# Kernel tuning notes

Hardware: AMD Instinct MI355X
Metric: run time of the kernel (lower is better)

The kernel has to match this reference:

```python
import math
import jax, jax.numpy as jnp
import numpy as np

B, N, F, FE = 16, 24, 128, 128   # crystals, atoms/crystal, atom feat, edge feat
NUM_Z = 100                       # num_atomic_numbers
GAUSS_STOP, BASIS_W = 6.0, 1.0
RADIUS_RATE = 1.0
N_CONV, N_FC, FC_F = 3, 4, 128
REP = 1                           # PBC replication per axis (27 images); exact for our cells
ZDIM = 2 * F + FE


def setup_inputs() -> dict:
    key = jax.random.key(0)
    ks = jax.random.split(key, 12)
    # cubic cells with side length in [8, 10) Angstrom -> rep per axis is exactly 1
    L = 8.0 + 2.0 * jax.random.uniform(ks[0], (B,))
    cell = L[:, None, None] * jnp.eye(3, dtype=jnp.float32)          # [B,3,3]
    frac = jax.random.uniform(ks[1], (B, N, 3))
    pos = jnp.einsum('bnd,bde->bne', frac, cell).reshape(B * N, 3)   # [B*N,3]
    atomic_numbers = jax.random.randint(ks[2], (B * N,), 1, NUM_Z + 1)
    batch = jnp.repeat(jnp.arange(B), N)
    emb = jax.random.normal(ks[3], (NUM_Z, F)) * 0.1                 # embedding table
    s = 1.0 / math.sqrt(ZDIM)
    conv_Wf = jax.random.normal(ks[4], (N_CONV, ZDIM, F)) * s
    conv_bf = jnp.zeros((N_CONV, F))
    conv_Ws = jax.random.normal(ks[5], (N_CONV, ZDIM, F)) * s
    conv_bs = jnp.zeros((N_CONV, F))
    sf = 1.0 / math.sqrt(FC_F)
    fc_W = jax.random.normal(ks[6], (N_FC - 1, FC_F, FC_F)) * sf
    fc_b = jnp.zeros((N_FC - 1, FC_F))
    W_out = jax.random.normal(ks[7], (FC_F, 1)) * sf
    b_out = jnp.zeros((1,))
    return {'pos': pos, 'cell': cell, 'emb': emb,
            'conv_Wf': conv_Wf, 'conv_bf': conv_bf,
            'conv_Ws': conv_Ws, 'conv_bs': conv_bs,
            'fc_W': fc_W, 'fc_b': fc_b, 'W_out': W_out, 'b_out': b_out,
            'atomic_numbers': atomic_numbers, 'batch': batch}


def _spectral_normalize(W, iters=5, eps=1e-12):
    # power iteration; sigma differentiable through W only (u,v detached) as in torch
    u = jnp.ones((W.shape[1],), W.dtype)
    u = u / jnp.linalg.norm(u)
    for _ in range(iters):
        v = W @ u
        v = v / (jnp.linalg.norm(v) + eps)
        u = W.T @ v
        u = u / (jnp.linalg.norm(u) + eps)
    u = jax.lax.stop_gradient(u)
    v = jax.lax.stop_gradient(v)
    sigma = v @ (W @ u)
    return W / sigma


def _forward(pos, cell, emb, conv_Wf, conv_bf, conv_Ws, conv_bs,
             fc_W, fc_b, W_out, b_out, atomic_numbers):
    # ---- graph construction (PBC all-pairs, fixed 27 images, masked) ----
    r = jnp.arange(-REP, REP + 1, dtype=cell.dtype)
    grid = jnp.stack(jnp.meshgrid(r, r, r, indexing='ij'), -1).reshape(-1, 3)  # [27,3]
    pbc = jnp.einsum('cd,bde->bce', grid, cell)                                # [B,27,3]
    posb = pos.reshape(B, N, 3)
    # disp[b,i,j,c] = pos_i - (pos_j + offset_c)
    disp = posb[:, :, None, None, :] - (posb[:, None, :, None, :] + pbc[:, None, None, :, :])
    dsqr = jnp.sum(disp * disp, -1)                                            # [B,N,N,27]
    cross = jnp.cross(cell[:, 1], cell[:, 2])
    vol = jnp.sum(cell[:, 0] * cross, -1)
    radius = RADIUS_RATE * (jnp.abs(vol) / N) ** (1.0 / 3.0)                   # [B]
    rb = radius[:, None, None, None]
    mask = (dsqr <= rb * rb) & (dsqr > 1e-4)
    dist = jnp.sqrt(jnp.maximum(dsqr, 1e-12))
    mf = mask.astype(pos.dtype)
    edge_w = (jnp.cos(dist * math.pi / rb) + 1.0) * mf                         # [B,N,N,27]
    # GaussianSmearing
    goff = jnp.linspace(0.0, GAUSS_STOP, FE)
    coeff = -0.5 / (BASIS_W * (goff[1] - goff[0])) ** 2
    edge_attr = jnp.exp(coeff * (dist[..., None] - goff) ** 2)                 # [B,N,N,27,FE]

    # ---- node features ----
    feat = jnp.tanh(emb[atomic_numbers - 1]).reshape(B, N, F)

    # ---- continuous graph convs (CGCNN-style gated conv, edge_weight scaled) ----
    for l in range(N_CONV):
        Wf, Ws = conv_Wf[l], conv_Ws[l]
        gi = feat @ Wf[:F]; gj = feat @ Wf[F:2 * F]
        ge = jnp.einsum('bijce,ef->bijcf', edge_attr, Wf[2 * F:])
        g = jax.nn.sigmoid(gi[:, :, None, None, :] + gj[:, None, :, None, :] + ge + conv_bf[l])
        si = feat @ Ws[:F]; sj = feat @ Ws[F:2 * F]
        se = jnp.einsum('bijce,ef->bijcf', edge_attr, Ws[2 * F:])
        sc = jax.nn.softplus(si[:, :, None, None, :] + sj[:, None, :, None, :] + se + conv_bs[l])
        msg = g * sc * edge_w[..., None]                                       # [B,N,N,27,F]
        feat = jax.nn.softplus(feat + msg.sum((2, 3)))                         # aggregate at i

    # ---- global mean pool + spectral-norm MLP head ----
    h = feat.mean(1)                                                           # [B,F]
    for l in range(N_FC - 1):
        h = jax.nn.softplus(h @ _spectral_normalize(fc_W[l]) + fc_b[l])
    return h @ W_out + b_out                                                   # [B,1]


def reference(pos, cell, emb, conv_Wf, conv_bf, conv_Ws, conv_bs,
              fc_W, fc_b, W_out, b_out, atomic_numbers, batch):
    return _forward(pos, cell, emb, conv_Wf, conv_bf, conv_Ws, conv_bs,
                    fc_W, fc_b, W_out, b_out, atomic_numbers)
```

## Files before the change

### kernel.cpp

```cpp
#include <hip/hip_runtime.h>
#include <math.h>

#define NB 16
#define NN 24
#define NA 384
#define FF 128
#define CC 27
#define MAXNBR 32

__device__ float g_sigma[4];
__device__ float g_projA[NA*4*FF];
__device__ float g_projB[NA*4*FF];
__device__ float g_feat [NA*FF];
__device__ __align__(128) int g_ctr[4*NB][32];
__device__ __align__(128) int g_sigdone[32];
__device__ __align__(128) int g_batchdone[32];

__device__ __forceinline__ float softplusf(float x){ return fmaxf(x,0.f) + log1pf(expf(-fabsf(x))); }
__device__ __forceinline__ float sigmoidf(float x){ return 1.f/(1.f+expf(-x)); }
__device__ __forceinline__ void st_agent(float* p, float v){
  __hip_atomic_store(p, v, __ATOMIC_RELAXED, __HIP_MEMORY_SCOPE_AGENT);
}
__device__ __forceinline__ float ld_agent(const float* p){
  return __hip_atomic_load(p, __ATOMIC_RELAXED, __HIP_MEMORY_SCOPE_AGENT);
}

__device__ __forceinline__ void band_dot(float dist, const float* __restrict__ Wf2,
                                         const float* __restrict__ Ws2, int f,
                                         float& ge, float& se)
{
  const float step  = 6.0f/127.0f;
  const float coeff = -0.5f/(step*step);
  int kmin = (int)ceilf(dist/step - 9.0f);
  kmin = kmin < 0 ? 0 : (kmin > 108 ? 108 : kmin);
  float g = 0.f, s = 0.f;
  #pragma unroll
  for (int t = 0; t < 20; t++) {
    int k = kmin + t;
    float dd = dist - step*(float)k;
    float a  = expf(coeff*dd*dd);
    g += a * Wf2[k*FF+f];
    s += a * Ws2[k*FF+f];
  }
  ge = g; se = s;
}

__device__ __forceinline__ float gemv_q(const float* __restrict__ Wf,
                                        const float* __restrict__ Ws,
                                        const float* s_ft, int q, int f)
{
  const float* W = (q==0) ? Wf : (q==1) ? (Wf + FF*FF) : (q==2) ? Ws : (Ws + FF*FF);
  float s = 0.f;
  #pragma unroll 16
  for (int k = 0; k < FF; k++) s += s_ft[k]*W[k*FF+f];
  return s;
}

__device__ __forceinline__ void publish(int* ctr)
{
  asm volatile("s_waitcnt vmcnt(0)" ::: "memory");
  __syncthreads();
  if (threadIdx.x == 0)
    __hip_atomic_fetch_add(ctr, 1, __ATOMIC_RELAXED, __HIP_MEMORY_SCOPE_AGENT);
}

__device__ __forceinline__ void wait_ge(int* ctr, int target)
{
  if (threadIdx.x == 0) {
    int guard = 0;
    while (__hip_atomic_load(ctr, __ATOMIC_RELAXED, __HIP_MEMORY_SCOPE_AGENT) < target) {
      __builtin_amdgcn_s_sleep(4);
      if (++guard > (1<<18)) break;
    }
  }
  __syncthreads();
}

__device__ __forceinline__ void edge_layer(int l, int q, int f, int n, int i,
       const float* __restrict__ projSrc,
       const float* __restrict__ conv_Wf, const float* __restrict__ conv_bf,
       const float* __restrict__ conv_Ws, const float* __restrict__ conv_bs,
       const int* s_nj, const float* s_nd, const float* s_nw,
       float (*s_p)[FF], float (*sm)[FF], float* s_ft)
{
  const float* Wf2 = conv_Wf + l*3*FF*FF + 2*FF*FF;
  const float* Ws2 = conv_Ws + l*3*FF*FF + 2*FF*FF;
  const float gi  = s_p[0][f];
  const float si  = s_p[2][f];
  const float bff = conv_bf[l*FF+f];
  const float bsf = conv_bs[l*FF+f];
  float msg = 0.f;
  for (int e = q; e < n; e += 4) {
    const int   jg   = s_nj[e];
    const float dist = s_nd[e];
    const float w    = s_nw[e];
    const float gj   = ld_agent(&projSrc[(jg*4+1)*FF+f]);
    const float sj   = ld_agent(&projSrc[(jg*4+3)*FF+f]);
    float ge, se;
    band_dot(dist, Wf2, Ws2, f, ge, se);
    msg += sigmoidf(gi + gj + ge + bff) * softplusf(si + sj + se + bsf) * w;
  }
  sm[q][f] = msg;
  __syncthreads();
  if (threadIdx.x < FF) {
    float v = softplusf(s_ft[f] + sm[0][f] + sm[1][f] + sm[2][f] + sm[3][f]);
    s_ft[f] = v;
  }
  __syncthreads();
}

__global__ void __launch_bounds__(512, 4)
k_fused(const float* __restrict__ pos, const float* __restrict__ cell,
        const float* __restrict__ emb,
        const float* __restrict__ conv_Wf, const float* __restrict__ conv_bf,
        const float* __restrict__ conv_Ws, const float* __restrict__ conv_bs,
        const float* __restrict__ fc_W,  const float* __restrict__ fc_b,
        const float* __restrict__ W_out, const float* __restrict__ b_out,
        const int* __restrict__ z, float* __restrict__ out)
{
  const int tid = threadIdx.x;
  const int q = tid >> 7, f = tid & 127;

  if (blockIdx.x < 3) {
    const int m = blockIdx.x;
    const float* W = fc_W + m*FF*FF;
    __shared__ float s_u[FF], s_v[FF], s_red2[FF];
    __shared__ float s_part2[4][FF];
    if (tid < FF) s_u[tid] = 0.08838834764831845f;
    __syncthreads();
    for (int it = 0; it < 5; it++) {
      { float p = 0.f;
        #pragma unroll
        for (int k = q*32; k < q*32+32; k++) p += W[f*FF+k]*s_u[k];
        s_part2[q][f] = p; }
      __syncthreads();
      if (tid < FF) { float s = s_part2[0][f]+s_part2[1][f]+s_part2[2][f]+s_part2[3][f];
                      s_v[f] = s; s_red2[f] = s*s; }
      __syncthreads();
      for (int st=64; st>0; st>>=1){ if (tid<st) s_red2[tid]+=s_red2[tid+st]; __syncthreads(); }
      float nv = sqrtf(s_red2[0]) + 1e-12f;
      __syncthreads();
      if (tid < FF) s_v[f] /= nv;
      __syncthreads();
      { float p = 0.f;
        #pragma unroll
        for (int r = q*32; r < q*32+32; r++) p += W[r*FF+f]*s_v[r];
        s_part2[q][f] = p; }
      __syncthreads();
      if (tid < FF) { float s = s_part2[0][f]+s_part2[1][f]+s_part2[2][f]+s_part2[3][f];
                      s_u[f] = s; s_red2[f] = s*s; }
      __syncthreads();
      for (int st=64; st>0; st>>=1){ if (tid<st) s_red2[tid]+=s_red2[tid+st]; __syncthreads(); }
      float nu = sqrtf(s_red2[0]) + 1e-12f;
      __syncthreads();
      if (tid < FF) s_u[f] /= nu;
      __syncthreads();
    }
    { float p = 0.f;
      #pragma unroll
      for (int k = q*32; k < q*32+32; k++) p += W[f*FF+k]*s_u[k];
      s_part2[q][f] = p; }
    __syncthreads();
    if (tid < FF) s_red2[f] = s_v[f]*(s_part2[0][f]+s_part2[1][f]+s_part2[2][f]+s_part2[3][f]);
    __syncthreads();
    for (int st=64; st>0; st>>=1){ if (tid<st) s_red2[tid]+=s_red2[tid+st]; __syncthreads(); }
    if (tid == 0) {
      st_agent(&g_sigma[m], s_red2[0]);
      asm volatile("s_waitcnt vmcnt(0)" ::: "memory");
      __hip_atomic_fetch_add(&g_sigdone[0], 1, __ATOMIC_RELAXED, __HIP_MEMORY_SCOPE_AGENT);
    }
    return;
  }

  const int i = (int)blockIdx.x - 3;
  const int b = i / NN;

  __shared__ float s_ft[FF];
  __shared__ float s_cell[9];
  __shared__ float s_rb;
  __shared__ int   s_cnt;
  __shared__ int   s_nj[MAXNBR];
  __shared__ float s_nd[MAXNBR];
  __shared__ float s_nw[MAXNBR];
  __shared__ float s_p[4][FF];
  __shared__ float sm[4][FF];
  __shared__ int   s_last;
  __shared__ float s_hh[FF], s_tmp[FF], s_red[FF];

  if (tid < FF) {
    int zi = z[i]; if (zi < 1) zi = 1; if (zi > 100) zi = 100;
    s_ft[tid] = tanhf(emb[(zi-1)*FF+tid]);
  }
  if (tid >= 256 && tid < 265) s_cell[tid-256] = cell[b*9 + tid - 256];
  if (tid == 500) s_cnt = 0;
  __syncthreads();
  if (tid == 0) {
    const float* c = s_cell;
    float cx = c[4]*c[8] - c[5]*c[7];
    float cy = c[5]*c[6] - c[3]*c[8];
    float cz = c[3]*c[7] - c[4]*c[6];
    float vol = c[0]*cx + c[1]*cy + c[2]*cz;
    s_rb = cbrtf(fabsf(vol)/(float)NN);
  }
  __syncthreads();
  {
    const float rb = s_rb, rb2 = rb*rb;
    const float pix = pos[i*3+0], piy = pos[i*3+1], piz = pos[i*3+2];
    const float PI = 3.14159265358979323846f;
    for (int cand = tid; cand < NN*CC; cand += 512) {
      int j = cand / CC, c = cand - j*CC;
      float gx = (float)(c/9) - 1.0f;
      float gy = (float)((c/3)%3) - 1.0f;
      float gz = (float)(c%3) - 1.0f;
      float ox = gx*s_cell[0] + gy*s_cell[3] + gz*s_cell[6];
      float oy = gx*s_cell[1] + gy*s_cell[4] + gz*s_cell[7];
      float oz = gx*s_cell[2] + gy*s_cell[5] + gz*s_cell[8];
      int jg = b*NN + j;
      float dx = pix - (pos[jg*3+0] + ox);
      float dy = piy - (pos[jg*3+1] + oy);
      float dz = piz - (pos[jg*3+2] + oz);
      float d2 = dx*dx + dy*dy + dz*dz;
      if (d2 <= rb2 && d2 > 1e-4f) {
        float dist = sqrtf(fmaxf(d2, 1e-4f));
        float w = cosf(dist*PI/rb) + 1.0f;
        int slot = atomicAdd(&s_cnt, 1);
        if (slot < MAXNBR) { s_nj[slot] = jg; s_nd[slot] = dist; s_nw[slot] = w; }
      }
    }
  }
  __syncthreads();
  const int n = (s_cnt > MAXNBR) ? MAXNBR : s_cnt;

  { float s0 = gemv_q(conv_Wf, conv_Ws, s_ft, q, f);
    s_p[q][f] = s0;
    st_agent(&g_projA[(i*4+q)*FF+f], s0); }
  publish(&g_ctr[0*NB+b][0]);
  wait_ge(&g_ctr[0*NB+b][0], NN);

  edge_layer(0, q, f, n, i, g_projA, conv_Wf, conv_bf, conv_Ws, conv_bs,
             s_nj, s_nd, s_nw, s_p, sm, s_ft);
  { float s1 = gemv_q(conv_Wf + 3*FF*FF, conv_Ws + 3*FF*FF, s_ft, q, f);
    s_p[q][f] = s1;
    st_agent(&g_projB[(i*4+q)*FF+f], s1); }
  publish(&g_ctr[1*NB+b][0]);
  wait_ge(&g_ctr[1*NB+b][0], NN);

  edge_layer(1, q, f, n, i, g_projB, conv_Wf, conv_bf, conv_Ws, conv_bs,
             s_nj, s_nd, s_nw, s_p, sm, s_ft);
  { float s2 = gemv_q(conv_Wf + 2*3*FF*FF, conv_Ws + 2*3*FF*FF, s_ft, q, f);
    s_p[q][f] = s2;
    st_agent(&g_projA[(i*4+q)*FF+f], s2); }
  publish(&g_ctr[2*NB+b][0]);
  wait_ge(&g_ctr[2*NB+b][0], NN);

  edge_layer(2, q, f, n, i, g_projA, conv_Wf, conv_bf, conv_Ws, conv_bs,
             s_nj, s_nd, s_nw, s_p, sm, s_ft);
  if (tid < FF) st_agent(&g_feat[i*FF+f], s_ft[f]);
  asm volatile("s_waitcnt vmcnt(0)" ::: "memory");
  __syncthreads();
  if (tid == 0)
    s_last = __hip_atomic_fetch_add(&g_ctr[3*NB+b][0], 1, __ATOMIC_RELAXED,
                                    __HIP_MEMORY_SCOPE_AGENT);
  __syncthreads();
  if (s_last != NN-1) return;

  if (tid == 0) {
    int guard = 0;
    while (__hip_atomic_load(&g_sigdone[0], __ATOMIC_RELAXED, __HIP_MEMORY_SCOPE_AGENT) < 3) {
      __builtin_amdgcn_s_sleep(4);
      if (++guard > (1<<18)) break;
    }
  }
  __syncthreads();
  if (tid < FF) {
    float s0 = 0.f;
    for (int a = 0; a < NN; a++) s0 += ld_agent(&g_feat[(b*NN+a)*FF+tid]);
    s_hh[tid] = s0/(float)NN;
  }
  __syncthreads();
  for (int l = 0; l < 3; l++) {
    { float p = 0.f;
      #pragma unroll
      for (int k = q*32; k < q*32+32; k++) p += s_hh[k]*fc_W[l*FF*FF + k*FF + f];
      sm[q][f] = p; }
    __syncthreads();
    if (tid < FF) {
      float s = sm[0][tid]+sm[1][tid]+sm[2][tid]+sm[3][tid];
      s_tmp[tid] = softplusf(s/ld_agent(&g_sigma[l]) + fc_b[l*FF+tid]);
    }
    __syncthreads();
    if (tid < FF) s_hh[tid] = s_tmp[tid];
    __syncthreads();
  }
  if (tid < FF) s_red[tid] = s_hh[tid]*W_out[tid];
  __syncthreads();
  if (tid < 64) {
    float t = s_red[tid] + s_red[tid+64];
    #pragma unroll
    for (int off = 32; off > 0; off >>= 1) t += __shfl_xor(t, off);
    if (tid == 0) {
      out[b] = t + b_out[0];
      __hip_atomic_store(&g_ctr[0*NB+b][0], 0, __ATOMIC_RELAXED, __HIP_MEMORY_SCOPE_AGENT);
      __hip_atomic_store(&g_ctr[1*NB+b][0], 0, __ATOMIC_RELAXED, __HIP_MEMORY_SCOPE_AGENT);
      __hip_atomic_store(&g_ctr[2*NB+b][0], 0, __ATOMIC_RELAXED, __HIP_MEMORY_SCOPE_AGENT);
      __hip_atomic_store(&g_ctr[3*NB+b][0], 0, __ATOMIC_RELAXED, __HIP_MEMORY_SCOPE_AGENT);
      int d = __hip_atomic_fetch_add(&g_batchdone[0], 1, __ATOMIC_RELAXED,
                                     __HIP_MEMORY_SCOPE_AGENT);
      if (d == NB-1) {
        __hip_atomic_store(&g_batchdone[0], 0, __ATOMIC_RELAXED, __HIP_MEMORY_SCOPE_AGENT);
        __hip_atomic_store(&g_sigdone[0],   0, __ATOMIC_RELAXED, __HIP_MEMORY_SCOPE_AGENT);
      }
    }
  }
}

extern "C" void kernel_launch(void* const* d_in, const int* in_sizes, int n_in,
                              void* d_out, int out_size, void* d_ws, size_t ws_size,
                              hipStream_t stream) {
  const float* pos     = (const float*)d_in[0];
  const float* cell    = (const float*)d_in[1];
  const float* emb     = (const float*)d_in[2];
  const float* conv_Wf = (const float*)d_in[3];
  const float* conv_bf = (const float*)d_in[4];
  const float* conv_Ws = (const float*)d_in[5];
  const float* conv_bs = (const float*)d_in[6];
  const float* fc_W    = (const float*)d_in[7];
  const float* fc_b    = (const float*)d_in[8];
  const float* W_out   = (const float*)d_in[9];
  const float* b_out   = (const float*)d_in[10];
  const int*   z       = (const int*)d_in[11];

  k_fused<<<NA+3, 512, 0, stream>>>(pos, cell, emb, conv_Wf, conv_bf,
                                    conv_Ws, conv_bs, fc_W, fc_b,
                                    W_out, b_out, z, (float*)d_out);
}
```

Measured before the change: 146.4 us.

## Precompute Gaussian edge bands and overlap edge projections with inter-block waits

Computes the Gaussian basis values once per edge into shared memory instead of recomputing the exponentials in every layer and feature lane. The per-edge edge-feature projections are now computed before waiting on the per-crystal barrier, so that work hides the synchronization latency. It also spreads that work evenly across all 512 threads rather than splitting edges four ways. It caps edges at 24 instead of 32, which could drop neighbors if a cell ever has more. Shared memory use grows, which may lower occupancy.

```diff
diff --git a/kernel.cpp b/kernel.cpp
--- a/kernel.cpp
+++ b/kernel.cpp
@@ -7,6 +7,8 @@
 #define FF 128
 #define CC 27
 #define MAXNBR 32
+#define MAXE 24
+#define NT 20
 
 __device__ float g_sigma[4];
 __device__ float g_projA[NA*4*FF];
@@ -25,20 +27,16 @@
   return __hip_atomic_load(p, __ATOMIC_RELAXED, __HIP_MEMORY_SCOPE_AGENT);
 }
 
-__device__ __forceinline__ void band_dot(float dist, const float* __restrict__ Wf2,
-                                         const float* __restrict__ Ws2, int f,
-                                         float& ge, float& se)
-{
-  const float step  = 6.0f/127.0f;
-  const float coeff = -0.5f/(step*step);
-  int kmin = (int)ceilf(dist/step - 9.0f);
-  kmin = kmin < 0 ? 0 : (kmin > 108 ? 108 : kmin);
+__device__ __forceinline__ void band_dot2(const float* __restrict__ ga, int kmin,
+                                          const float* __restrict__ Wf2,
+                                          const float* __restrict__ Ws2, int f,
+                                          float& ge, float& se)
+{
   float g = 0.f, s = 0.f;
   #pragma unroll
-  for (int t = 0; t < 20; t++) {
+  for (int t = 0; t < NT; t++) {
+    float a = ga[t];
     int k = kmin + t;
-    float dd = dist - step*(float)k;
-    float a  = expf(coeff*dd*dd);
     g += a * Wf2[k*FF+f];
     s += a * Ws2[k*FF+f];
   }
@@ -72,39 +70,6 @@
       __builtin_amdgcn_s_sleep(4);
       if (++guard > (1<<18)) break;
     }
-  }
-  __syncthreads();
-}
-
-__device__ __forceinline__ void edge_layer(int l, int q, int f, int n, int i,
-       const float* __restrict__ projSrc,
-       const float* __restrict__ conv_Wf, const float* __restrict__ conv_bf,
-       const float* __restrict__ conv_Ws, const float* __restrict__ conv_bs,
-       const int* s_nj, const float* s_nd, const float* s_nw,
-       float (*s_p)[FF], float (*sm)[FF], float* s_ft)
-{
-  const float* Wf2 = conv_Wf + l*3*FF*FF + 2*FF*FF;
-  const float* Ws2 = conv_Ws + l*3*FF*FF + 2*FF*FF;
-  const float gi  = s_p[0][f];
-  const float si  = s_p[2][f];
-  const float bff = conv_bf[l*FF+f];
-  const float bsf = conv_bs[l*FF+f];
-  float msg = 0.f;
-  for (int e = q; e < n; e += 4) {
-    const int   jg   = s_nj[e];
-    const float dist = s_nd[e];
-    const float w    = s_nw[e];
-    const float gj   = ld_agent(&projSrc[(jg*4+1)*FF+f]);
-    const float sj   = ld_agent(&projSrc[(jg*4+3)*FF+f]);
-    float ge, se;
-    band_dot(dist, Wf2, Ws2, f, ge, se);
-    msg += sigmoidf(gi + gj + ge + bff) * softplusf(si + sj + se + bsf) * w;
-  }
-  sm[q][f] = msg;
-  __syncthreads();
-  if (threadIdx.x < FF) {
-    float v = softplusf(s_ft[f] + sm[0][f] + sm[1][f] + sm[2][f] + sm[3][f]);
-    s_ft[f] = v;
   }
   __syncthreads();
 }
@@ -121,60 +86,6 @@
   const int tid = threadIdx.x;
   const int q = tid >> 7, f = tid & 127;
 
-  if (blockIdx.x < 3) {
-    const int m = blockIdx.x;
-    const float* W = fc_W + m*FF*FF;
-    __shared__ float s_u[FF], s_v[FF], s_red2[FF];
-    __shared__ float s_part2[4][FF];
-    if (tid < FF) s_u[tid] = 0.08838834764831845f;
-    __syncthreads();
-    for (int it = 0; it < 5; it++) {
-      { float p = 0.f;
-        #pragma unroll
-        for (int k = q*32; k < q*32+32; k++) p += W[f*FF+k]*s_u[k];
-        s_part2[q][f] = p; }
-      __syncthreads();
-      if (tid < FF) { float s = s_part2[0][f]+s_part2[1][f]+s_part2[2][f]+s_part2[3][f];
-                      s_v[f] = s; s_red2[f] = s*s; }
-      __syncthreads();
-      for (int st=64; st>0; st>>=1){ if (tid<st) s_red2[tid]+=s_red2[tid+st]; __syncthreads(); }
-      float nv = sqrtf(s_red2[0]) + 1e-12f;
-      __syncthreads();
-      if (tid < FF) s_v[f] /= nv;
-      __syncthreads();
-      { float p = 0.f;
-        #pragma unroll
-        for (int r = q*32; r < q*32+32; r++) p += W[r*FF+f]*s_v[r];
-        s_part2[q][f] = p; }
-      __syncthreads();
-      if (tid < FF) { float s = s_part2[0][f]+s_part2[1][f]+s_part2[2][f]+s_part2[3][f];
-                      s_u[f] = s; s_red2[f] = s*s; }
-      __syncthreads();
-      for (int st=64; st>0; st>>=1){ if (tid<st) s_red2[tid]+=s_red2[tid+st]; __syncthreads(); }
-      float nu = sqrtf(s_red2[0]) + 1e-12f;
-      __syncthreads();
-      if (tid < FF) s_u[f] /= nu;
-      __syncthreads();
-    }
-    { float p = 0.f;
-      #pragma unroll
-      for (int k = q*32; k < q*32+32; k++) p += W[f*FF+k]*s_u[k];
-      s_part2[q][f] = p; }
-    __syncthreads();
-    if (tid < FF) s_red2[f] = s_v[f]*(s_part2[0][f]+s_part2[1][f]+s_part2[2][f]+s_part2[3][f]);
-    __syncthreads();
-    for (int st=64; st>0; st>>=1){ if (tid<st) s_red2[tid]+=s_red2[tid+st]; __syncthreads(); }
-    if (tid == 0) {
-      st_agent(&g_sigma[m], s_red2[0]);
-      asm volatile("s_waitcnt vmcnt(0)" ::: "memory");
-      __hip_atomic_fetch_add(&g_sigdone[0], 1, __ATOMIC_RELAXED, __HIP_MEMORY_SCOPE_AGENT);
-    }
-    return;
-  }
-
-  const int i = (int)blockIdx.x - 3;
-  const int b = i / NN;
-
   __shared__ float s_ft[FF];
   __shared__ float s_cell[9];
   __shared__ float s_rb;
@@ -182,10 +93,66 @@
   __shared__ int   s_nj[MAXNBR];
   __shared__ float s_nd[MAXNBR];
   __shared__ float s_nw[MAXNBR];
+  __shared__ float s_ga[MAXE][NT];
+  __shared__ int   s_km[MAXE];
+  __shared__ float s_ge[MAXE][FF];
+  __shared__ float s_se[MAXE][FF];
   __shared__ float s_p[4][FF];
   __shared__ float sm[4][FF];
   __shared__ int   s_last;
   __shared__ float s_hh[FF], s_tmp[FF], s_red[FF];
+
+  if (blockIdx.x < 3) {
+    const int m = blockIdx.x;
+    const float* W = fc_W + m*FF*FF;
+    if (tid < FF) s_hh[tid] = 0.08838834764831845f;
+    __syncthreads();
+    for (int it = 0; it < 5; it++) {
+      { float p = 0.f;
+        #pragma unroll
+        for (int k = q*32; k < q*32+32; k++) p += W[f*FF+k]*s_hh[k];
+        sm[q][f] = p; }
+      __syncthreads();
+      if (tid < FF) { float s = sm[0][f]+sm[1][f]+sm[2][f]+sm[3][f];
+                      s_tmp[f] = s; s_red[f] = s*s; }
+      __syncthreads();
+      for (int st=64; st>0; st>>=1){ if (tid<st) s_red[tid]+=s_red[tid+st]; __syncthreads(); }
+      float nv = sqrtf(s_red[0]) + 1e-12f;
+      __syncthreads();
+      if (tid < FF) s_tmp[f] /= nv;
+      __syncthreads();
+      { float p = 0.f;
+        #pragma unroll
+        for (int r = q*32; r < q*32+32; r++) p += W[r*FF+f]*s_tmp[r];
+        sm[q][f] = p; }
+      __syncthreads();
+      if (tid < FF) { float s = sm[0][f]+sm[1][f]+sm[2][f]+sm[3][f];
+                      s_hh[f] = s; s_red[f] = s*s; }
+      __syncthreads();
+      for (int st=64; st>0; st>>=1){ if (tid<st) s_red[tid]+=s_red[tid+st]; __syncthreads(); }
+      float nu = sqrtf(s_red[0]) + 1e-12f;
+      __syncthreads();
+      if (tid < FF) s_hh[f] /= nu;
+      __syncthreads();
+    }
+    { float p = 0.f;
+      #pragma unroll
+      for (int k = q*32; k < q*32+32; k++) p += W[f*FF+k]*s_hh[k];
+      sm[q][f] = p; }
+    __syncthreads();
+    if (tid < FF) s_red[f] = s_tmp[f]*(sm[0][f]+sm[1][f]+sm[2][f]+sm[3][f]);
+    __syncthreads();
+    for (int st=64; st>0; st>>=1){ if (tid<st) s_red[tid]+=s_red[tid+st]; __syncthreads(); }
+    if (tid == 0) {
+      st_agent(&g_sigma[m], s_red[0]);
+      asm volatile("s_waitcnt vmcnt(0)" ::: "memory");
+      __hip_atomic_fetch_add(&g_sigdone[0], 1, __ATOMIC_RELAXED, __HIP_MEMORY_SCOPE_AGENT);
+    }
+    return;
+  }
+
+  const int i = (int)blockIdx.x - 3;
+  const int b = i / NN;
 
   if (tid < FF) {
     int zi = z[i]; if (zi < 1) zi = 1; if (zi > 100) zi = 100;
@@ -229,33 +196,72 @@
     }
   }
   __syncthreads();
-  const int n = (s_cnt > MAXNBR) ? MAXNBR : s_cnt;
+  const int n0 = (s_cnt > MAXNBR) ? MAXNBR : s_cnt;
+  const int n  = (n0 > MAXE) ? MAXE : n0;
+
+  for (int idx = tid; idx < n*NT; idx += 512) {
+    int e = idx / NT, t = idx - e*NT;
+    float dist = s_nd[e];
+    const float step  = 6.0f/127.0f;
+    const float coeff = -0.5f/(step*step);
+    int kmin = (int)ceilf(dist/step - 9.0f);
+    kmin = kmin < 0 ? 0 : (kmin > 108 ? 108 : kmin);
+    if (t == 0) s_km[e] = kmin;
+    int k = kmin + t;
+    float dd = dist - step*(float)k;
+    s_ga[e][t] = expf(coeff*dd*dd);
+  }
+  __syncthreads();
 
   { float s0 = gemv_q(conv_Wf, conv_Ws, s_ft, q, f);
     s_p[q][f] = s0;
     st_agent(&g_projA[(i*4+q)*FF+f], s0); }
   publish(&g_ctr[0*NB+b][0]);
-  wait_ge(&g_ctr[0*NB+b][0], NN);
-
-  edge_layer(0, q, f, n, i, g_projA, conv_Wf, conv_bf, conv_Ws, conv_bs,
-             s_nj, s_nd, s_nw, s_p, sm, s_ft);
-  { float s1 = gemv_q(conv_Wf + 3*FF*FF, conv_Ws + 3*FF*FF, s_ft, q, f);
-    s_p[q][f] = s1;
-    st_agent(&g_projB[(i*4+q)*FF+f], s1); }
-  publish(&g_ctr[1*NB+b][0]);
-  wait_ge(&g_ctr[1*NB+b][0], NN);
-
-  edge_layer(1, q, f, n, i, g_projB, conv_Wf, conv_bf, conv_Ws, conv_bs,
-             s_nj, s_nd, s_nw, s_p, sm, s_ft);
-  { float s2 = gemv_q(conv_Wf + 2*3*FF*FF, conv_Ws + 2*3*FF*FF, s_ft, q, f);
-    s_p[q][f] = s2;
-    st_agent(&g_projA[(i*4+q)*FF+f], s2); }
-  publish(&g_ctr[2*NB+b][0]);
-  wait_ge(&g_ctr[2*NB+b][0], NN);
-
-  edge_layer(2, q, f, n, i, g_projA, conv_Wf, conv_bf, conv_Ws, conv_bs,
-             s_nj, s_nd, s_nw, s_p, sm, s_ft);
-  if (tid < FF) st_agent(&g_feat[i*FF+f], s_ft[f]);
+
+  for (int l = 0; l < 3; ++l) {
+    const float* projSrc = (l==1) ? g_projB : g_projA;
+    const float* Wf2 = conv_Wf + l*3*FF*FF + 2*FF*FF;
+    const float* Ws2 = conv_Ws + l*3*FF*FF + 2*FF*FF;
+    for (int idx = tid; idx < n*FF; idx += 512) {
+      int e = idx >> 7, ff = idx & 127;
+      float ge, se;
+      band_dot2(&s_ga[e][0], s_km[e], Wf2, Ws2, ff, ge, se);
+      s_ge[e][ff] = ge; s_se[e][ff] = se;
+    }
+    __syncthreads();
+    wait_ge(&g_ctr[l*NB+b][0], NN);
+    {
+      const float gi = s_p[0][f], si = s_p[2][f];
+      const float bff = conv_bf[l*FF+f], bsf = conv_bs[l*FF+f];
+      float msg = 0.f;
+      for (int e = q; e < n; e += 4) {
+        int   jg = s_nj[e];
+        float w  = s_nw[e];
+        float gj = ld_agent(&projSrc[(jg*4+1)*FF+f]);
+        float sj = ld_agent(&projSrc[(jg*4+3)*FF+f]);
+        msg += sigmoidf(gi + gj + s_ge[e][f] + bff)
+             * softplusf(si + sj + s_se[e][f] + bsf) * w;
+      }
+      sm[q][f] = msg;
+    }
+    __syncthreads();
+    if (tid < FF) {
+      s_ft[tid] = softplusf(s_ft[tid] + sm[0][tid] + sm[1][tid]
+                                      + sm[2][tid] + sm[3][tid]);
+    }
+    __syncthreads();
+    if (l < 2) {
+      const float* WfN = conv_Wf + (l+1)*3*FF*FF;
+      const float* WsN = conv_Ws + (l+1)*3*FF*FF;
+      float* projDst = (l==0) ? g_projB : g_projA;
+      float s1 = gemv_q(WfN, WsN, s_ft, q, f);
+      s_p[q][f] = s1;
+      st_agent(&projDst[(i*4+q)*FF+f], s1);
+      publish(&g_ctr[(l+1)*NB+b][0]);
+    }
+  }
+
+  if (tid < FF) st_agent(&g_feat[i*FF+tid], s_ft[tid]);
   asm volatile("s_waitcnt vmcnt(0)" ::: "memory");
   __syncthreads();
   if (tid == 0)
```

Result: faster. 135.8 us (-7.2%).
